# Kernel tuning notes

Hardware: AMD Instinct MI355X
Metric: run time of the kernel (lower is better)

Reference implementation:

```python
import jax, jax.numpy as jnp
import numpy as np

HEADS = 16
EMBED_DIM = 1024
HEAD_DIM = EMBED_DIM // HEADS
N, Q_LEN, KV_LEN = 4, 2048, 2048


def setup_inputs() -> dict:
    key = jax.random.key(0)
    k1, k2, k3, k4, k5, k6 = jax.random.split(key, 6)
    query = jax.random.normal(k1, (N, Q_LEN, EMBED_DIM), dtype=jnp.float32)
    key_t = jax.random.normal(k2, (N, KV_LEN, EMBED_DIM), dtype=jnp.float32)
    value = jax.random.normal(k3, (N, KV_LEN, EMBED_DIM), dtype=jnp.float32)
    mask = jax.random.randint(k4, (N, 1, Q_LEN, KV_LEN), 0, 2, dtype=jnp.int32)
    # output projection (the only Linear actually used in the original forward)
    W_out = jax.random.normal(k5, (EMBED_DIM, EMBED_DIM), dtype=jnp.float32) / np.sqrt(EMBED_DIM)
    b_out = jax.random.normal(k6, (EMBED_DIM,), dtype=jnp.float32) * 0.01
    return {"query": query, "key": key_t, "value": value, "mask": mask,
            "W_out": W_out, "b_out": b_out}


def reference(query, key, value, mask, W_out, b_out):
    n, q_len, _ = query.shape
    k_len = key.shape[1]
    # split heads: [N, L, E] -> [N, L, H, D]
    q = query.reshape(n, q_len, HEADS, HEAD_DIM)
    k = key.reshape(n, k_len, HEADS, HEAD_DIM)
    v = value.reshape(n, k_len, HEADS, HEAD_DIM)
    # full QK^T scores: [N, H, Q, K]
    scores = jnp.einsum("nqhd,nkhd->nhqk", q, k)
    scores = jnp.where(mask == 0, jnp.float32(-1e9), scores)
    # non-canonical scale: 1/sqrt(embed_dim), applied AFTER masking (as original)
    attn = jax.nn.softmax(scores / jnp.sqrt(jnp.float32(EMBED_DIM)), axis=3)
    out = jnp.einsum("nhql,nlhd->nqhd", attn, v).reshape(n, q_len, HEADS * HEAD_DIM)
    return out @ W_out.T + b_out
```

## Files before the change

kernel.cpp:

```cpp
#include <hip/hip_runtime.h>
#include <stdint.h>

#define NB 4
#define QL 2048
#define KL 2048
#define HEADS 16
#define EMB 1024
#define HD 64

typedef float f32x4 __attribute__((ext_vector_type(4)));
typedef float f32x16 __attribute__((ext_vector_type(16)));
typedef __bf16 bf16x8 __attribute__((ext_vector_type(8)));
typedef unsigned short u16x8 __attribute__((ext_vector_type(8)));
typedef unsigned short u16x4 __attribute__((ext_vector_type(4)));
typedef unsigned int u32x4 __attribute__((ext_vector_type(4)));

static __device__ __forceinline__ unsigned short f2bf(float f) {
  unsigned u = __float_as_uint(f);
  u += 0x7fffu + ((u >> 16) & 1u);
  return (unsigned short)(u >> 16);
}
static __device__ __forceinline__ float bf2f(unsigned short h) {
  return __uint_as_float(((unsigned)h) << 16);
}
static __device__ __forceinline__ unsigned int rnebits(float f) {
  unsigned u = __float_as_uint(f);
  return u + 0x7fffu + ((u >> 16) & 1u);
}
static __device__ __forceinline__ unsigned int pack_bf2(float a, float b) {
  return __builtin_amdgcn_perm(rnebits(a), rnebits(b), 0x03020706u);
}
static __device__ __forceinline__ void dma16(const void* g, void* l) {
  __builtin_amdgcn_global_load_lds(
      (const __attribute__((address_space(1))) unsigned int*)(uintptr_t)g,
      (__attribute__((address_space(3))) unsigned int*)(uintptr_t)l, 16, 0, 0);
}

#define XHI_OFF  0ull
#define XLO_OFF  16777216ull
#define KHI_OFF  33554432ull
#define VT_OFF   50331648ull
#define WHI_OFF  67108864ull
#define WLO_OFF  69206016ull
#define MB_OFF   71303168ull

#define QSC  0.0450842399f
#define ESHIFT 11.5415601730f

__global__ __launch_bounds__(256) void prep_all(const float* __restrict__ Kg,
                                                const float* __restrict__ Vg,
                                                const float* __restrict__ Wg,
                                                const int* __restrict__ Mg,
                                                unsigned short* __restrict__ Khi,
                                                unsigned short* __restrict__ Vt,
                                                unsigned short* __restrict__ Whi,
                                                unsigned short* __restrict__ Wlo,
                                                unsigned long long* __restrict__ bits) {
  __shared__ unsigned short lds[64 * 66];
  const int tid = threadIdx.x;
  const int bid = blockIdx.x;
  if (bid < 8192) {
    int t = bid * 256 + tid;
    int d4 = t & 15, h = (t >> 4) & 15, kv = (t >> 8) & 2047, n = t >> 19;
    f32x4 a = *(const f32x4*)(Kg + (size_t)(n * KL + kv) * EMB + h * 64 + d4 * 4);
    u16x4 o;
    #pragma unroll
    for (int j = 0; j < 4; ++j) o[j] = f2bf(a[j]);
    int row = kv & 63, c0 = d4 >> 1;
    int pos = row * 128 + ((c0 ^ (row & 7)) << 4) + (d4 & 1) * 8;
    size_t slab = (size_t)((n * 16 + h) * 32 + (kv >> 6)) * 8192;
    *(u16x4*)((char*)Khi + slab + pos) = o;
  } else if (bid < 10240) {
    int vb = bid - 8192;
    int kt = vb & 31, h = (vb >> 5) & 15, n = vb >> 9;
    #pragma unroll
    for (int i = 0; i < 4; ++i) {
      int e = i * 256 + tid;
      int d4 = e & 15, kvl = e >> 4;
      int col = (kvl & 48) | (kvl & 3) | ((kvl & 4) << 1) | ((kvl & 8) >> 1);
      f32x4 a = *(const f32x4*)(Vg + (size_t)(n * KL + kt * 64 + kvl) * EMB + h * 64 + d4 * 4);
      #pragma unroll
      for (int j = 0; j < 4; ++j) lds[(d4 * 4 + j) * 66 + col] = f2bf(a[j]);
    }
    __syncthreads();
    size_t slab = (size_t)((n * 16 + h) * 32 + kt) * 8192;
    #pragma unroll
    for (int i = 0; i < 4; ++i) {
      int e = i * 256 + tid;
      int kv4 = e & 15, d = e >> 4;
      u16x4 o;
      #pragma unroll
      for (int j = 0; j < 4; ++j) o[j] = lds[d * 66 + kv4 * 4 + j];
      int c0 = kv4 >> 1;
      int pos = d * 128 + ((c0 ^ (d & 7)) << 4) + (kv4 & 1) * 8;
      *(u16x4*)((char*)Vt + slab + pos) = o;
    }
  } else if (bid < 11264) {
    int t = (bid - 10240) * 256 + tid;
    int c4 = t & 255, row = t >> 8;
    f32x4 a = *(const f32x4*)(Wg + (size_t)row * 1024 + c4 * 4);
    u16x4 hi, lo;
    #pragma unroll
    for (int j = 0; j < 4; ++j) {
      unsigned short hb = f2bf(a[j]);
      hi[j] = hb;
      lo[j] = f2bf(a[j] - bf2f(hb));
    }
    *(u16x4*)(Whi + (size_t)row * 1024 + c4 * 4) = hi;
    *(u16x4*)(Wlo + (size_t)row * 1024 + c4 * 4) = lo;
  } else {
    int t = (bid - 11264) * 256 + tid;
    int w = t >> 6, lane = t & 63;
    int row = w >> 5, kw = w & 31;
    int v = Mg[row * KL + kw * 64 + lane];
    unsigned long long b = __ballot(v != 0);
    if (lane == 0) bits[w] = b;
  }
}

__global__ __launch_bounds__(256, 4) void attn2(const float* __restrict__ Qg,
                                                const unsigned short* __restrict__ Khi,
                                                const unsigned short* __restrict__ Vt,
                                                const unsigned long long* __restrict__ mb,
                                                unsigned short* __restrict__ Xhi,
                                                unsigned short* __restrict__ Xlo) {
  __shared__ __align__(16) char smem[16384];
  const int tid = threadIdx.x;
  const int w = tid >> 6;
  const int l = tid & 63;
  const int q32 = l & 31;
  const int h5 = l >> 5;
  const int bid = blockIdx.x;
  const int qb = bid & 15;
  const int h = (bid >> 4) & 15;
  const int n = bid >> 8;
  const int q0 = qb * 128 + w * 32;

  const char* kslab = (const char*)Khi + (size_t)(n * HEADS + h) * 262144;
  const char* vslab = (const char*)Vt + (size_t)(n * HEADS + h) * 262144;

  bf16x8 qh[4];
  {
    const float* qp = Qg + (size_t)(n * QL + q0 + q32) * EMB + h * HD + h5 * 8;
    #pragma unroll
    for (int kc = 0; kc < 4; ++kc) {
      union { u16x8 u; bf16x8 b; } H;
      #pragma unroll
      for (int j = 0; j < 8; ++j) H.u[j] = f2bf(qp[kc * 16 + j] * QSC);
      qh[kc] = H.b;
    }
  }

  int kaddr[2][4], vaddr[2][4];
  #pragma unroll
  for (int Mt = 0; Mt < 2; ++Mt) {
    int row = Mt * 32 + q32;
    #pragma unroll
    for (int g = 0; g < 4; ++g) {
      kaddr[Mt][g] = row * 128 + (((g * 2 + h5) ^ (row & 7)) << 4);
      vaddr[Mt][g] = 8192 + row * 128 + (((g * 2 + h5) ^ (row & 7)) << 4);
    }
  }

  f32x16 o0, o1;
  #pragma unroll
  for (int i = 0; i < 16; ++i) { o0[i] = 0.f; o1[i] = 0.f; }
  float lsA = 0.f, lsB = 0.f;

  const unsigned long long* mrow = mb + (size_t)(n * QL + q0 + q32) * 32;
  const int soff = tid * 16;

  for (int kt = 0; kt < 32; ++kt) {
    __syncthreads();
    dma16(kslab + kt * 8192 + soff,        smem + w * 1024);
    dma16(kslab + kt * 8192 + 4096 + soff, smem + 4096 + w * 1024);
    dma16(vslab + kt * 8192 + soff,        smem + 8192 + w * 1024);
    dma16(vslab + kt * 8192 + 4096 + soff, smem + 12288 + w * 1024);
    __syncthreads();

    uint2 mw = *(const uint2*)(mrow + kt);

    #pragma unroll
    for (int Mt = 0; Mt < 2; ++Mt) {
      f32x16 st;
      #pragma unroll
      for (int i = 0; i < 16; ++i) st[i] = 0.f;
      #pragma unroll
      for (int kc = 0; kc < 4; ++kc) {
        union { u16x8 u; bf16x8 b; } kf;
        kf.u = *(const u16x8*)(smem + kaddr[Mt][kc]);
        st = __builtin_amdgcn_mfma_f32_32x32x16_bf16(kf.b, qh[kc], st, 0, 0, 0);
      }
      unsigned int half = (Mt ? mw.y : mw.x) >> (h5 * 4);
      unsigned int pk[8];
      #pragma unroll
      for (int i = 0; i < 8; ++i) {
        const int r0 = 2 * i, r1 = 2 * i + 1;
        const int b0 = (r0 & 3) + 8 * (r0 >> 2);
        float a0 = st[r0] - ESHIFT;
        float a1 = st[r1] - ESHIFT;
        a0 = ((half >> b0) & 1u) ? a0 : -1.0e38f;
        a1 = ((half >> (b0 + 1)) & 1u) ? a1 : -1.0e38f;
        float p0 = exp2f(a0);
        float p1 = exp2f(a1);
        lsA += p0;
        lsB += p1;
        pk[i] = pack_bf2(p0, p1);
      }
      #pragma unroll
      for (int kc2 = 0; kc2 < 2; ++kc2) {
        union { u32x4 wv; bf16x8 b; } pf;
        pf.wv[0] = pk[4 * kc2 + 0];
        pf.wv[1] = pk[4 * kc2 + 1];
        pf.wv[2] = pk[4 * kc2 + 2];
        pf.wv[3] = pk[4 * kc2 + 3];
        const int kvc = Mt * 2 + kc2;
        union { u16x8 u; bf16x8 b; } vf0, vf1;
        vf0.u = *(const u16x8*)(smem + vaddr[0][kvc]);
        vf1.u = *(const u16x8*)(smem + vaddr[1][kvc]);
        o0 = __builtin_amdgcn_mfma_f32_32x32x16_bf16(pf.b, vf0.b, o0, 0, 0, 0);
        o1 = __builtin_amdgcn_mfma_f32_32x32x16_bf16(pf.b, vf1.b, o1, 0, 0, 0);
      }
    }
  }

  float lsum = lsA + lsB;
  lsum += __shfl_xor(lsum, 32);
  float invq = 1.0f / lsum;
  #pragma unroll
  for (int r = 0; r < 16; ++r) {
    int qr = (r & 3) + 8 * (r >> 2) + 4 * h5;
    float inv = __shfl(invq, qr, 32);
    size_t base = (size_t)(n * QL + q0 + qr) * EMB + h * HD + q32;
    float v0 = o0[r] * inv;
    unsigned short h0 = f2bf(v0);
    Xhi[base] = h0;
    Xlo[base] = f2bf(v0 - bf2f(h0));
    float v1 = o1[r] * inv;
    unsigned short h1 = f2bf(v1);
    Xhi[base + 32] = h1;
    Xlo[base + 32] = f2bf(v1 - bf2f(h1));
  }
}

__global__ __launch_bounds__(256) void proj2(const unsigned short* __restrict__ Xhi,
                                             const unsigned short* __restrict__ Xlo,
                                             const unsigned short* __restrict__ Whi,
                                             const unsigned short* __restrict__ Wlo,
                                             const float* __restrict__ bias,
                                             float* __restrict__ out) {
  __shared__ __align__(16) char pm[32768];
  const int tid = threadIdx.x;
  const int w = tid >> 6;
  const int l = tid & 63;
  const int lr = l & 15;
  const int lq = l >> 4;
  const int wm = w >> 1, wn = w & 1;
  const int bid = blockIdx.x;
  const int m0 = (bid >> 3) * 128;
  const int n0 = (bid & 7) * 128;

  f32x4 acc[4][4];
  #pragma unroll
  for (int i = 0; i < 4; ++i)
    #pragma unroll
    for (int j = 0; j < 4; ++j) acc[i][j] = (f32x4){0.f, 0.f, 0.f, 0.f};

  for (int kc = 0; kc < 32; ++kc) {
    __syncthreads();
    #pragma unroll
    for (int i = 0; i < 8; ++i) {
      int s = (i * 256 + tid) * 16;
      int sel = s >> 13;
      int s2 = s & 8191;
      int row = s2 >> 6;
      int c = (s2 >> 4) & 3;
      const unsigned short* pl = sel == 0 ? Xhi : sel == 1 ? Xlo : sel == 2 ? Whi : Wlo;
      int rbase = (sel < 2 ? m0 : n0) + row;
      dma16(pl + (size_t)rbase * 1024 + kc * 32 + c * 8, pm + i * 4096 + w * 1024);
    }
    __syncthreads();

    bf16x8 ah[4], al[4], bh[4], bl[4];
    #pragma unroll
    for (int mt = 0; mt < 4; ++mt) {
      int off = (wm * 64 + mt * 16 + lr) * 64 + lq * 16;
      union { u16x8 u; bf16x8 b; } A, B;
      A.u = *(const u16x8*)(pm + off);
      B.u = *(const u16x8*)(pm + 8192 + off);
      ah[mt] = A.b;
      al[mt] = B.b;
    }
    #pragma unroll
    for (int nt = 0; nt < 4; ++nt) {
      int off = (wn * 64 + nt * 16 + lr) * 64 + lq * 16;
      union { u16x8 u; bf16x8 b; } A, B;
      A.u = *(const u16x8*)(pm + 16384 + off);
      B.u = *(const u16x8*)(pm + 24576 + off);
      bh[nt] = A.b;
      bl[nt] = B.b;
    }
    #pragma unroll
    for (int mt = 0; mt < 4; ++mt)
      #pragma unroll
      for (int nt = 0; nt < 4; ++nt) {
        f32x4 c = acc[mt][nt];
        c = __builtin_amdgcn_mfma_f32_16x16x32_bf16(ah[mt], bh[nt], c, 0, 0, 0);
        c = __builtin_amdgcn_mfma_f32_16x16x32_bf16(ah[mt], bl[nt], c, 0, 0, 0);
        c = __builtin_amdgcn_mfma_f32_16x16x32_bf16(al[mt], bh[nt], c, 0, 0, 0);
        acc[mt][nt] = c;
      }
  }

  #pragma unroll
  for (int nt = 0; nt < 4; ++nt) {
    int col = n0 + wn * 64 + nt * 16 + lr;
    float bv = bias[col];
    #pragma unroll
    for (int mt = 0; mt < 4; ++mt) {
      int rowb = m0 + wm * 64 + mt * 16 + lq * 4;
      #pragma unroll
      for (int r = 0; r < 4; ++r)
        out[(size_t)(rowb + r) * EMB + col] = acc[mt][nt][r] + bv;
    }
  }
}

extern "C" void kernel_launch(void* const* d_in, const int* in_sizes, int n_in,
                              void* d_out, int out_size, void* d_ws, size_t ws_size,
                              hipStream_t stream) {
  const float* Qg = (const float*)d_in[0];
  const float* Kg = (const float*)d_in[1];
  const float* Vg = (const float*)d_in[2];
  const int* Mg = (const int*)d_in[3];
  const float* Wg = (const float*)d_in[4];
  const float* Bg = (const float*)d_in[5];
  float* out = (float*)d_out;

  char* ws = (char*)d_ws;
  unsigned short* xhi = (unsigned short*)(ws + XHI_OFF);
  unsigned short* xlo = (unsigned short*)(ws + XLO_OFF);
  unsigned short* khi = (unsigned short*)(ws + KHI_OFF);
  unsigned short* vt = (unsigned short*)(ws + VT_OFF);
  unsigned short* whi = (unsigned short*)(ws + WHI_OFF);
  unsigned short* wlo = (unsigned short*)(ws + WLO_OFF);
  unsigned long long* mbits = (unsigned long long*)(ws + MB_OFF);

  prep_all<<<76800, 256, 0, stream>>>(Kg, Vg, Wg, Mg, khi, vt, whi, wlo, mbits);
  attn2<<<NB * HEADS * (QL / 128), 256, 0, stream>>>(Qg, khi, vt, mbits, xhi, xlo);
  proj2<<<(NB * QL / 128) * (EMB / 128), 256, 0, stream>>>(xhi, xlo, whi, wlo, Bg, out);
}
```

Baseline: 381.7 us.

## Double-buffer attention and projection tiles with async LDS loads; stage mask bits

Both the attention and projection kernels now double-buffer their shared-memory tiles: the next K/V (or X/W) tile is issued via global_load_lds before the current tile is computed, with explicit vmcnt waits replacing the synchronous load/sync pattern. The mask bitmap is re-laid out in prep so each block streams its mask words into LDS alongside K/V. The softmax row sum is now computed by an extra MFMA against a ones vector, and the exp shift is folded into the accumulator init. Native exp2, rcp and bf16 conversion replace the hand-rolled versions. This doubles LDS use per block and adds one MFMA per PV step, which may reduce occupancy.

After: 345.2 us. 1.11x faster.

```diff
diff --git a/kernel.cpp b/kernel.cpp
--- a/kernel.cpp
+++ b/kernel.cpp
@@ -8,8 +8,10 @@
 #define EMB 1024
 #define HD 64
 
+typedef float f32x2 __attribute__((ext_vector_type(2)));
 typedef float f32x4 __attribute__((ext_vector_type(4)));
 typedef float f32x16 __attribute__((ext_vector_type(16)));
+typedef __bf16 bf16x2 __attribute__((ext_vector_type(2)));
 typedef __bf16 bf16x8 __attribute__((ext_vector_type(8)));
 typedef unsigned short u16x8 __attribute__((ext_vector_type(8)));
 typedef unsigned short u16x4 __attribute__((ext_vector_type(4)));
@@ -23,18 +25,36 @@
 static __device__ __forceinline__ float bf2f(unsigned short h) {
   return __uint_as_float(((unsigned)h) << 16);
 }
-static __device__ __forceinline__ unsigned int rnebits(float f) {
-  unsigned u = __float_as_uint(f);
-  return u + 0x7fffu + ((u >> 16) & 1u);
-}
-static __device__ __forceinline__ unsigned int pack_bf2(float a, float b) {
-  return __builtin_amdgcn_perm(rnebits(a), rnebits(b), 0x03020706u);
+static __device__ __forceinline__ float fast_exp2(float x) {
+#if __has_builtin(__builtin_amdgcn_exp2f)
+  return __builtin_amdgcn_exp2f(x);
+#else
+  return __expf(x * 0.6931471805599453f);
+#endif
+}
+static __device__ __forceinline__ float fast_rcp(float x) {
+#if __has_builtin(__builtin_amdgcn_rcpf)
+  return __builtin_amdgcn_rcpf(x);
+#else
+  return 1.0f / x;
+#endif
 }
 static __device__ __forceinline__ void dma16(const void* g, void* l) {
   __builtin_amdgcn_global_load_lds(
       (const __attribute__((address_space(1))) unsigned int*)(uintptr_t)g,
       (__attribute__((address_space(3))) unsigned int*)(uintptr_t)l, 16, 0, 0);
 }
+static __device__ __forceinline__ void dma4(const void* g, void* l) {
+  __builtin_amdgcn_global_load_lds(
+      (const __attribute__((address_space(1))) unsigned int*)(uintptr_t)g,
+      (__attribute__((address_space(3))) unsigned int*)(uintptr_t)l, 4, 0, 0);
+}
+static __device__ __forceinline__ void barrier_plain() {
+  __asm__ volatile("" ::: "memory");
+  __builtin_amdgcn_s_barrier();
+  __asm__ volatile("" ::: "memory");
+}
+#define WAITVM(N) __asm__ volatile("s_waitcnt vmcnt(" #N ")" ::: "memory")
 
 #define XHI_OFF  0ull
 #define XLO_OFF  16777216ull
@@ -110,21 +130,23 @@
     *(u16x4*)(Wlo + (size_t)row * 1024 + c4 * 4) = lo;
   } else {
     int t = (bid - 11264) * 256 + tid;
-    int w = t >> 6, lane = t & 63;
-    int row = w >> 5, kw = w & 31;
+    int wd = t >> 6, lane = t & 63;
+    int row = wd >> 5, kw = wd & 31;
     int v = Mg[row * KL + kw * 64 + lane];
     unsigned long long b = __ballot(v != 0);
-    if (lane == 0) bits[w] = b;
-  }
-}
-
-__global__ __launch_bounds__(256, 4) void attn2(const float* __restrict__ Qg,
+    int q = row & 2047, nn = row >> 11;
+    if (lane == 0)
+      bits[((size_t)((nn * 16 + (q >> 7)) * 32 + kw)) * 128 + (q & 127)] = b;
+  }
+}
+
+__global__ __launch_bounds__(256, 4) void attn3(const float* __restrict__ Qg,
                                                 const unsigned short* __restrict__ Khi,
                                                 const unsigned short* __restrict__ Vt,
-                                                const unsigned long long* __restrict__ mb,
+                                                const unsigned long long* __restrict__ Mb,
                                                 unsigned short* __restrict__ Xhi,
                                                 unsigned short* __restrict__ Xlo) {
-  __shared__ __align__(16) char smem[16384];
+  __shared__ __align__(16) char smem[2 * 17408];
   const int tid = threadIdx.x;
   const int w = tid >> 6;
   const int l = tid & 63;
@@ -138,6 +160,7 @@
 
   const char* kslab = (const char*)Khi + (size_t)(n * HEADS + h) * 262144;
   const char* vslab = (const char*)Vt + (size_t)(n * HEADS + h) * 262144;
+  const char* mslab = (const char*)Mb + (size_t)(n * 16 + qb) * 32768;
 
   bf16x8 qh[4];
   {
@@ -150,62 +173,70 @@
       qh[kc] = H.b;
     }
   }
-
-  int kaddr[2][4], vaddr[2][4];
-  #pragma unroll
-  for (int Mt = 0; Mt < 2; ++Mt) {
-    int row = Mt * 32 + q32;
-    #pragma unroll
-    for (int g = 0; g < 4; ++g) {
-      kaddr[Mt][g] = row * 128 + (((g * 2 + h5) ^ (row & 7)) << 4);
-      vaddr[Mt][g] = 8192 + row * 128 + (((g * 2 + h5) ^ (row & 7)) << 4);
-    }
-  }
-
-  f32x16 o0, o1;
-  #pragma unroll
-  for (int i = 0; i < 16; ++i) { o0[i] = 0.f; o1[i] = 0.f; }
-  float lsA = 0.f, lsB = 0.f;
-
-  const unsigned long long* mrow = mb + (size_t)(n * QL + q0 + q32) * 32;
-  const int soff = tid * 16;
-
-  for (int kt = 0; kt < 32; ++kt) {
-    __syncthreads();
-    dma16(kslab + kt * 8192 + soff,        smem + w * 1024);
-    dma16(kslab + kt * 8192 + 4096 + soff, smem + 4096 + w * 1024);
-    dma16(vslab + kt * 8192 + soff,        smem + 8192 + w * 1024);
-    dma16(vslab + kt * 8192 + 4096 + soff, smem + 12288 + w * 1024);
-    __syncthreads();
-
-    uint2 mw = *(const uint2*)(mrow + kt);
+  WAITVM(0);
+
+  int off8[2][4];
+  #pragma unroll
+  for (int r2 = 0; r2 < 2; ++r2)
+    #pragma unroll
+    for (int g = 0; g < 4; ++g)
+      off8[r2][g] = (r2 * 32 + q32) * 128 + (((2 * g + h5) ^ (q32 & 7)) << 4);
+
+  f32x16 o0, o1, ol;
+  #pragma unroll
+  for (int i = 0; i < 16; ++i) { o0[i] = 0.f; o1[i] = 0.f; ol[i] = 0.f; }
+
+  union { u16x8 u; bf16x8 b; } O1;
+  #pragma unroll
+  for (int j = 0; j < 8; ++j) O1.u[j] = 0x3F80;
+  const bf16x8 ones = O1.b;
+
+  auto issue = [&](int kt, char* buf) {
+    const char* ks = kslab + kt * 8192 + w * 2048 + l * 16;
+    const char* vs = vslab + kt * 8192 + w * 2048 + l * 16;
+    dma16(ks, buf + w * 2048);
+    dma16(ks + 1024, buf + w * 2048 + 1024);
+    dma16(vs, buf + 8192 + w * 2048);
+    dma16(vs + 1024, buf + 8192 + w * 2048 + 1024);
+    dma4(mslab + kt * 1024 + w * 256 + l * 4, buf + 16384 + w * 256);
+  };
+
+  auto step = [&](int kt, char* cur, char* nxt) {
+    barrier_plain();
+    if (kt != 31) {
+      issue(kt + 1, nxt);
+      WAITVM(5);
+    } else {
+      WAITVM(0);
+    }
+    barrier_plain();
+    uint2 mw = *(const uint2*)(cur + 16384 + w * 256 + q32 * 8);
 
     #pragma unroll
     for (int Mt = 0; Mt < 2; ++Mt) {
       f32x16 st;
       #pragma unroll
-      for (int i = 0; i < 16; ++i) st[i] = 0.f;
+      for (int i = 0; i < 16; ++i) st[i] = -ESHIFT;
       #pragma unroll
       for (int kc = 0; kc < 4; ++kc) {
         union { u16x8 u; bf16x8 b; } kf;
-        kf.u = *(const u16x8*)(smem + kaddr[Mt][kc]);
+        kf.u = *(const u16x8*)(cur + off8[Mt][kc]);
         st = __builtin_amdgcn_mfma_f32_32x32x16_bf16(kf.b, qh[kc], st, 0, 0, 0);
       }
       unsigned int half = (Mt ? mw.y : mw.x) >> (h5 * 4);
       unsigned int pk[8];
       #pragma unroll
       for (int i = 0; i < 8; ++i) {
-        const int r0 = 2 * i, r1 = 2 * i + 1;
+        const int r0 = 2 * i;
         const int b0 = (r0 & 3) + 8 * (r0 >> 2);
-        float a0 = st[r0] - ESHIFT;
-        float a1 = st[r1] - ESHIFT;
-        a0 = ((half >> b0) & 1u) ? a0 : -1.0e38f;
-        a1 = ((half >> (b0 + 1)) & 1u) ? a1 : -1.0e38f;
-        float p0 = exp2f(a0);
-        float p1 = exp2f(a1);
-        lsA += p0;
-        lsB += p1;
-        pk[i] = pack_bf2(p0, p1);
+        float a0 = ((half >> b0) & 1u) ? st[r0] : -1.0e38f;
+        float a1 = ((half >> (b0 + 1)) & 1u) ? st[r0 + 1] : -1.0e38f;
+        float p0 = fast_exp2(a0);
+        float p1 = fast_exp2(a1);
+        bf16x2 pv = __builtin_convertvector((f32x2){p0, p1}, bf16x2);
+        unsigned int u;
+        __builtin_memcpy(&u, &pv, 4);
+        pk[i] = u;
       }
       #pragma unroll
       for (int kc2 = 0; kc2 < 2; ++kc2) {
@@ -216,21 +247,25 @@
         pf.wv[3] = pk[4 * kc2 + 3];
         const int kvc = Mt * 2 + kc2;
         union { u16x8 u; bf16x8 b; } vf0, vf1;
-        vf0.u = *(const u16x8*)(smem + vaddr[0][kvc]);
-        vf1.u = *(const u16x8*)(smem + vaddr[1][kvc]);
+        vf0.u = *(const u16x8*)(cur + 8192 + off8[0][kvc]);
+        vf1.u = *(const u16x8*)(cur + 8192 + off8[1][kvc]);
         o0 = __builtin_amdgcn_mfma_f32_32x32x16_bf16(pf.b, vf0.b, o0, 0, 0, 0);
         o1 = __builtin_amdgcn_mfma_f32_32x32x16_bf16(pf.b, vf1.b, o1, 0, 0, 0);
+        ol = __builtin_amdgcn_mfma_f32_32x32x16_bf16(pf.b, ones, ol, 0, 0, 0);
       }
     }
-  }
-
-  float lsum = lsA + lsB;
-  lsum += __shfl_xor(lsum, 32);
-  float invq = 1.0f / lsum;
+  };
+
+  issue(0, smem);
+  for (int kt2 = 0; kt2 < 16; ++kt2) {
+    step(2 * kt2, smem, smem + 17408);
+    step(2 * kt2 + 1, smem + 17408, smem);
+  }
+
   #pragma unroll
   for (int r = 0; r < 16; ++r) {
+    float inv = fast_rcp(ol[r]);
     int qr = (r & 3) + 8 * (r >> 2) + 4 * h5;
-    float inv = __shfl(invq, qr, 32);
     size_t base = (size_t)(n * QL + q0 + qr) * EMB + h * HD + q32;
     float v0 = o0[r] * inv;
     unsigned short h0 = f2bf(v0);
@@ -243,13 +278,13 @@
   }
 }
 
-__global__ __launch_bounds__(256) void proj2(const unsigned short* __restrict__ Xhi,
-                                             const unsigned short* __restrict__ Xlo,
-                                             const unsigned short* __restrict__ Whi,
-                                             const unsigned short* __restrict__ Wlo,
-                                             const float* __restrict__ bias,
-                                             float* __restrict__ out) {
-  __shared__ __align__(16) char pm[32768];
+__global__ __launch_bounds__(256, 2) void proj3(const unsigned short* __restrict__ Xhi,
+                                                const unsigned short* __restrict__ Xlo,
+                                                const unsigned short* __restrict__ Whi,
+                                                const unsigned short* __restrict__ Wlo,
+                                                const float* __restrict__ bias,
+                                                float* __restrict__ out) {
+  __shared__ __align__(16) char pm[65536];
   const int tid = threadIdx.x;
   const int w = tid >> 6;
   const int l = tid & 63;
@@ -266,8 +301,7 @@
     #pragma unroll
     for (int j = 0; j < 4; ++j) acc[i][j] = (f32x4){0.f, 0.f, 0.f, 0.f};
 
-  for (int kc = 0; kc < 32; ++kc) {
-    __syncthreads();
+  auto issue = [&](int kc, char* buf) {
     #pragma unroll
     for (int i = 0; i < 8; ++i) {
       int s = (i * 256 + tid) * 16;
@@ -277,17 +311,27 @@
       int c = (s2 >> 4) & 3;
       const unsigned short* pl = sel == 0 ? Xhi : sel == 1 ? Xlo : sel == 2 ? Whi : Wlo;
       int rbase = (sel < 2 ? m0 : n0) + row;
-      dma16(pl + (size_t)rbase * 1024 + kc * 32 + c * 8, pm + i * 4096 + w * 1024);
-    }
-    __syncthreads();
+      dma16(pl + (size_t)rbase * 1024 + kc * 32 + c * 8, buf + i * 4096 + w * 1024);
+    }
+  };
+
+  auto pstep = [&](int kc, char* cur, char* nxt) {
+    barrier_plain();
+    if (kc != 31) {
+      issue(kc + 1, nxt);
+      WAITVM(8);
+    } else {
+      WAITVM(0);
+    }
+    barrier_plain();
 
     bf16x8 ah[4], al[4], bh[4], bl[4];
     #pragma unroll
     for (int mt = 0; mt < 4; ++mt) {
       int off = (wm * 64 + mt * 16 + lr) * 64 + lq * 16;
       union { u16x8 u; bf16x8 b; } A, B;
-      A.u = *(const u16x8*)(pm + off);
-      B.u = *(const u16x8*)(pm + 8192 + off);
+      A.u = *(const u16x8*)(cur + off);
+      B.u = *(const u16x8*)(cur + 8192 + off);
       ah[mt] = A.b;
       al[mt] = B.b;
     }
@@ -295,8 +339,8 @@
     for (int nt = 0; nt < 4; ++nt) {
       int off = (wn * 64 + nt * 16 + lr) * 64 + lq * 16;
       union { u16x8 u; bf16x8 b; } A, B;
-      A.u = *(const u16x8*)(pm + 16384 + off);
-      B.u = *(const u16x8*)(pm + 24576 + off);
+      A.u = *(const u16x8*)(cur + 16384 + off);
+      B.u = *(const u16x8*)(cur + 24576 + off);
       bh[nt] = A.b;
       bl[nt] = B.b;
     }
@@ -310,6 +354,12 @@
         c = __builtin_amdgcn_mfma_f32_16x16x32_bf16(al[mt], bh[nt], c, 0, 0, 0);
         acc[mt][nt] = c;
       }
+  };
+
+  issue(0, pm);
+  for (int kc2 = 0; kc2 < 16; ++kc2) {
+    pstep(2 * kc2, pm, pm + 32768);
+    pstep(2 * kc2 + 1, pm + 32768, pm);
   }
 
   #pragma unroll
@@ -347,6 +397,6 @@
   unsigned long long* mbits = (unsigned long long*)(ws + MB_OFF);
 
   prep_all<<<76800, 256, 0, stream>>>(Kg, Vg, Wg, Mg, khi, vt, whi, wlo, mbits);
-  attn2<<<NB * HEADS * (QL / 128), 256, 0, stream>>>(Qg, khi, vt, mbits, xhi, xlo);
-  proj2<<<(NB * QL / 128) * (EMB / 128), 256, 0, stream>>>(xhi, xlo, whi, wlo, Bg, out);
-}
+  attn3<<<NB * HEADS * (QL / 128), 256, 0, stream>>>(Qg, khi, vt, mbits, xhi, xlo);
+  proj3<<<(NB * QL / 128) * (EMB / 128), 256, 0, stream>>>(xhi, xlo, whi, wlo, Bg, out);
+}
```
